# Performance work log

Measured on AMD Instinct MI355X. Metric: run time of the kernel, lower is better.

Reference implementation:

```python
import jax, jax.numpy as jnp
import numpy as np

D_MODEL = 1024
D_STATE = 16
D_CONV = 4
EXPAND = 2
D_INNER = D_MODEL * EXPAND
BATCH = 2
SEQ = 1024


def setup_inputs() -> dict:
    key = jax.random.key(0)
    ks = jax.random.split(key, 9)
    s = lambda fan: 1.0 / np.sqrt(fan)
    x = jax.random.normal(ks[0], (BATCH, SEQ, D_MODEL), jnp.float32)
    W_in = jax.random.normal(ks[1], (D_MODEL, 2 * D_INNER), jnp.float32) * s(D_MODEL)
    conv_w = jax.random.normal(ks[2], (D_INNER, 1, D_CONV), jnp.float32) * s(D_CONV)
    conv_b = jax.random.normal(ks[3], (D_INNER,), jnp.float32) * 0.01
    W_xproj = jax.random.normal(ks[4], (D_INNER, 2 * D_STATE + 1), jnp.float32) * s(D_INNER)
    W_dt = jax.random.normal(ks[5], (1, D_INNER), jnp.float32)
    dt_std = 1.0 / np.sqrt(D_INNER)
    b_dt = jax.random.uniform(ks[6], (D_INNER,), jnp.float32, minval=-dt_std, maxval=dt_std)
    A_log = jnp.log(jnp.arange(1, D_STATE + 1, dtype=jnp.float32))
    Dp = jnp.ones((D_INNER,), jnp.float32)
    W_out = jax.random.normal(ks[7], (D_INNER, D_MODEL), jnp.float32) * s(D_INNER)
    return dict(x=x, W_in=W_in, conv_w=conv_w, conv_b=conv_b, W_xproj=W_xproj,
                W_dt=W_dt, b_dt=b_dt, A_log=A_log, Dp=Dp, W_out=W_out)


def _mamba_forward(x, W_in, conv_w, conv_b, W_xproj, W_dt, b_dt, A_log, Dp, W_out):
    # input projection, split into x branch and gate z
    xz = x @ W_in                              # (B, L, 2*d_inner)
    x_in, z = jnp.split(xz, 2, axis=-1)
    # causal depthwise conv1d: left-pad d_conv-1 (equiv to torch pad=d_conv-1 + truncate to L)
    xc = jnp.transpose(x_in, (0, 2, 1))        # (B, d_inner, L)
    xc = jax.lax.conv_general_dilated(
        xc, conv_w, window_strides=(1,), padding=[(D_CONV - 1, 0)],
        feature_group_count=D_INNER, dimension_numbers=('NCH', 'OIH', 'NCH'))
    xc = xc + conv_b[None, :, None]
    xc = jax.nn.silu(jnp.transpose(xc, (0, 2, 1)))  # (B, L, d_inner)
    # selective SSM
    A = -jnp.exp(A_log)                        # (N,)
    xp = xc @ W_xproj                          # (B, L, 2N+1)
    dt_raw = xp[..., :1]                       # (B, L, 1)
    B_sel = xp[..., 1:1 + D_STATE]             # (B, L, N)
    C_sel = xp[..., 1 + D_STATE:]              # (B, L, N)
    delta = jax.nn.softplus(dt_raw @ W_dt + b_dt)       # (B, L, d_inner)
    dA = jnp.exp(delta[..., None] * A)                   # (B, L, d, N)
    dBx = (delta * xc)[..., None] * B_sel[:, :, None, :]  # (B, L, d, N)

    def step(h, inp):
        dA_t, dBx_t, C_t = inp                 # (B,d,N),(B,d,N),(B,N)
        h = dA_t * h + dBx_t
        y_t = jnp.einsum('bdn,bn->bd', h, C_t)
        return h, y_t

    h0 = jnp.zeros((x.shape[0], D_INNER, D_STATE), xc.dtype)
    _, ys = jax.lax.scan(step, h0,
                         (dA.swapaxes(0, 1), dBx.swapaxes(0, 1), C_sel.swapaxes(0, 1)))
    y = ys.swapaxes(0, 1) + Dp * xc            # (B, L, d_inner)
    y = y * jax.nn.silu(z)
    return y @ W_out                           # (B, L, d_model)


def reference(x, W_in, conv_w, conv_b, W_xproj, W_dt, b_dt, A_log, Dp, W_out):
    return _mamba_forward(x, W_in, conv_w, conv_b, W_xproj, W_dt, b_dt, A_log, Dp, W_out)
```

## Files before the change

### kernel.cpp

```cpp
#include <hip/hip_runtime.h>


#define NTOK   2048
#define NC     64
#define TC     16

typedef unsigned short u16;
typedef short short8 __attribute__((ext_vector_type(8)));
typedef float f32x4 __attribute__((ext_vector_type(4)));

__device__ __forceinline__ float bf2f(u16 v) {
    union { unsigned int u; float f; } w; w.u = ((unsigned int)v) << 16; return w.f;
}
__device__ __forceinline__ u16 f2bf(float f) {
    union { float f; unsigned int u; } w; w.f = f;
    unsigned int u = w.u;
    return (u16)((u + 0x7fffu + ((u >> 16) & 1u)) >> 16);
}

__device__ __forceinline__ void gload_lds16(const u16* g, u16* l) {
    __builtin_amdgcn_global_load_lds(
        (const __attribute__((address_space(1))) void*)g,
        (__attribute__((address_space(3))) void*)l, 16, 0, 0);
}

__device__ __forceinline__ float softplus_f(float x) {
    return fmaxf(x, 0.f) + __logf(1.f + __expf(-__builtin_fabsf(x)));
}

__device__ __forceinline__ void transpose_tile(const float* __restrict__ in,
                                               u16* __restrict__ out,
                                               int R, int C, int n0, int k0,
                                               int tid) {
    __shared__ float tile[32][33];
    const int tx = tid & 31, ty = tid >> 5;
    #pragma unroll
    for (int i = 0; i < 32; i += 8)
        tile[ty + i][tx] = in[(size_t)(k0 + ty + i) * C + n0 + tx];
    __syncthreads();
    #pragma unroll
    for (int i = 0; i < 32; i += 8)
        out[(size_t)(n0 + ty + i) * R + k0 + tx] = f2bf(tile[tx][ty + i]);
}

__global__ __launch_bounds__(256)
void prep_all(const float* __restrict__ x, const float* __restrict__ W_in,
              const float* __restrict__ W_out, const float* __restrict__ W_xproj,
              u16* __restrict__ xbf, u16* __restrict__ WinT,
              u16* __restrict__ WoutT, u16* __restrict__ WxpT) {
    const int tid = threadIdx.x;
    int blk = blockIdx.x;
    if (blk < 8192) {
        int i = blk * 256 + tid;
        xbf[i] = f2bf(x[i]);
        return;
    }
    blk -= 8192;
    if (blk < 4096) {
        transpose_tile(W_in, WinT, 1024, 4096, (blk & 127) * 32, (blk >> 7) * 32, tid);
        return;
    }
    blk -= 4096;
    if (blk < 2048) {
        transpose_tile(W_out, WoutT, 2048, 1024, (blk & 31) * 32, (blk >> 5) * 32, tid);
        return;
    }
    blk -= 2048;
    {
        int gid = blk * 256 + tid;
        int k = gid & 2047;
        int n = gid >> 11;
        WxpT[(size_t)n * 2048 + k] = (n < 33) ? f2bf(W_xproj[(size_t)k * 33 + n]) : (u16)0;
    }
}

template <int OUT_MODE>
__global__ __launch_bounds__(256)
void gemm_bt(const u16* __restrict__ A, const u16* __restrict__ Bt,
             void* __restrict__ Cv, int M, int N, int K) {
    __shared__ __align__(16) u16 As[128 * 32];
    __shared__ __align__(16) u16 Bs[128 * 32];

    const int tid  = threadIdx.x;
    const int lane = tid & 63;
    const int w    = tid >> 6;
    const int wm   = (w >> 1) * 64;
    const int wn   = (w & 1) * 64;
    const int r    = lane & 15;
    const int q    = lane >> 4;
    const int m0   = blockIdx.x * 128;
    const int n0   = blockIdx.y * 128;
    const int kChunk = K / gridDim.z;
    const int k0   = blockIdx.z * kChunk;

    f32x4 acc[4][4];
    #pragma unroll
    for (int i = 0; i < 4; ++i)
        #pragma unroll
        for (int j = 0; j < 4; ++j)
            acc[i][j] = (f32x4){0.f, 0.f, 0.f, 0.f};

    for (int kk = k0; kk < k0 + kChunk; kk += 32) {
        __syncthreads();
        #pragma unroll
        for (int i = 0; i < 2; ++i) {
            int c   = tid + i * 256;
            int row = c >> 2;
            int kc  = (c & 3) << 3;
            int wb  = (i * 256 + (tid & 192)) * 8;
            gload_lds16(&A[(size_t)(m0 + row) * K + kk + kc], &As[wb]);
            gload_lds16(&Bt[(size_t)(n0 + row) * K + kk + kc], &Bs[wb]);
        }
        __syncthreads();

        short8 af[4], bf[4];
        #pragma unroll
        for (int mt = 0; mt < 4; ++mt)
            af[mt] = *(const short8*)(&As[(wm + mt * 16 + r) * 32 + q * 8]);
        #pragma unroll
        for (int nt = 0; nt < 4; ++nt)
            bf[nt] = *(const short8*)(&Bs[(wn + nt * 16 + r) * 32 + q * 8]);

        #pragma unroll
        for (int mt = 0; mt < 4; ++mt)
            #pragma unroll
            for (int nt = 0; nt < 4; ++nt)
                acc[mt][nt] = __builtin_amdgcn_mfma_f32_16x16x32_bf16(
                    af[mt], bf[nt], acc[mt][nt], 0, 0, 0);
    }

    #pragma unroll
    for (int mt = 0; mt < 4; ++mt) {
        #pragma unroll
        for (int nt = 0; nt < 4; ++nt) {
            #pragma unroll
            for (int i = 0; i < 4; ++i) {
                int row = m0 + wm + mt * 16 + q * 4 + i;
                int col = n0 + wn + nt * 16 + r;
                float v = acc[mt][nt][i];
                size_t idx = (size_t)row * N + col;
                if (OUT_MODE == 0) {
                    ((float*)Cv)[idx] = v;
                } else if (OUT_MODE == 1) {
                    atomicAdd(&((float*)Cv)[idx], v);
                } else {
                    ((u16*)Cv)[idx] = f2bf(v);
                }
            }
        }
    }
}

__global__ __launch_bounds__(256)
void conv_silu(const u16* __restrict__ xz, const float* __restrict__ cw,
               const float* __restrict__ cb, u16* __restrict__ xcb) {
    const int d   = blockIdx.x * 256 + threadIdx.x;
    const int tok = blockIdx.y;
    const int b   = tok >> 10;
    const int t   = tok & 1023;
    float s = cb[d];
    #pragma unroll
    for (int k = 0; k < 4; ++k) {
        int tt = t - 3 + k;
        if (tt >= 0)
            s += bf2f(xz[(size_t)(b * 1024 + tt) * 4096 + d]) * cw[d * 4 + k];
    }
    float sl = s / (1.f + __expf(-s));
    xcb[(size_t)tok * 2048 + d] = f2bf(sl);
}

__device__ __forceinline__ void pow_tree(float e1, float* dA) {
    float e2 = e1 * e1, e4 = e2 * e2, e8 = e4 * e4;
    dA[0] = e1;       dA[1] = e2;       dA[2] = e2 * e1;  dA[3] = e4;
    dA[4] = e4 * e1;  dA[5] = e4 * e2;  dA[6] = e4 * dA[2]; dA[7] = e8;
    dA[8] = e8 * e1;  dA[9] = e8 * e2;  dA[10] = e8 * dA[2]; dA[11] = e8 * e4;
    dA[12] = e8 * dA[4]; dA[13] = e8 * dA[5]; dA[14] = e8 * dA[6]; dA[15] = e8 * e8;
}

__global__ __launch_bounds__(256)
void scan_pass1(const u16* __restrict__ xcb, const float* __restrict__ xp,
                const float* __restrict__ W_dt, const float* __restrict__ b_dt,
                const float* __restrict__ A_log,
                float* __restrict__ Sdl, float* __restrict__ hend) {
    const int c  = blockIdx.x;
    const int dg = blockIdx.y;
    const int b  = blockIdx.z;
    const int tid = threadIdx.x;
    const int d  = dg * 256 + tid;
    const int tok0 = b * 1024 + c * TC;

    __shared__ float xps[TC][36];
    for (int e = tid; e < TC * 33; e += 256) {
        int t = (e * 993) >> 15;
        int j = e - t * 33;
        xps[t][j] = xp[(size_t)(tok0 + t) * 128 + j];
    }
    __syncthreads();

    float a[16];
    bool fast = true;
    #pragma unroll
    for (int n = 0; n < 16; ++n) {
        a[n] = -__expf(A_log[n]);
        fast = fast && (__builtin_fabsf(a[n] + (float)(n + 1)) < 1e-3f * (n + 1));
    }

    const float wdt = W_dt[d];
    const float bdt = b_dt[d];

    float h[16];
    #pragma unroll
    for (int n = 0; n < 16; ++n) h[n] = 0.f;
    float sdl = 0.f;

    for (int t = 0; t < TC; ++t) {
        const int tok = tok0 + t;
        const float dl = softplus_f(xps[t][0] * wdt + bdt);
        sdl += dl;
        const float xv = bf2f(xcb[(size_t)tok * 2048 + d]);
        const float wv = dl * xv;
        if (fast) {
            float dA[16];
            pow_tree(__expf(-dl), dA);
            #pragma unroll
            for (int n = 0; n < 16; ++n)
                h[n] = fmaf(dA[n], h[n], wv * xps[t][1 + n]);
        } else {
            #pragma unroll
            for (int n = 0; n < 16; ++n)
                h[n] = fmaf(__expf(dl * a[n]), h[n], wv * xps[t][1 + n]);
        }
    }

    Sdl[(size_t)(b * NC + c) * 2048 + d] = sdl;
    #pragma unroll
    for (int n = 0; n < 16; ++n)
        hend[((size_t)((b * NC + c) * 16 + n)) * 2048 + d] = h[n];
}

__global__ __launch_bounds__(256)
void scan_combine(const float* __restrict__ Sdl, const float* __restrict__ A_log,
                  float* __restrict__ hend) {
    const int gid = blockIdx.x * 256 + threadIdx.x;
    const int d = gid & 2047;
    const int n = (gid >> 11) & 15;
    const int b = gid >> 15;
    const float an = -__expf(A_log[n]);
    float H = 0.f;
    for (int c = 0; c < NC; ++c) {
        size_t cidx = (size_t)(b * NC + c);
        float s  = Sdl[cidx * 2048 + d];
        size_t idx = (cidx * 16 + n) * 2048 + d;
        float he = hend[idx];
        hend[idx] = H;
        H = fmaf(__expf(an * s), H, he);
    }
}

__global__ __launch_bounds__(256)
void scan_pass2(const u16* __restrict__ xcb, const float* __restrict__ xp,
                const float* __restrict__ W_dt, const float* __restrict__ b_dt,
                const float* __restrict__ A_log, const float* __restrict__ Hstart,
                const float* __restrict__ Dp, const u16* __restrict__ xz,
                u16* __restrict__ ybuf) {
    const int c  = blockIdx.x;
    const int dg = blockIdx.y;
    const int b  = blockIdx.z;
    const int tid = threadIdx.x;
    const int d  = dg * 256 + tid;
    const int tok0 = b * 1024 + c * TC;

    __shared__ float xps[TC][36];
    for (int e = tid; e < TC * 33; e += 256) {
        int t = (e * 993) >> 15;
        int j = e - t * 33;
        xps[t][j] = xp[(size_t)(tok0 + t) * 128 + j];
    }
    __syncthreads();

    float a[16];
    bool fast = true;
    #pragma unroll
    for (int n = 0; n < 16; ++n) {
        a[n] = -__expf(A_log[n]);
        fast = fast && (__builtin_fabsf(a[n] + (float)(n + 1)) < 1e-3f * (n + 1));
    }

    const float wdt = W_dt[d];
    const float bdt = b_dt[d];

    float h[16];
    #pragma unroll
    for (int n = 0; n < 16; ++n)
        h[n] = Hstart[((size_t)((b * NC + c) * 16 + n)) * 2048 + d];

    const float Dd = Dp[d];
    for (int t = 0; t < TC; ++t) {
        const int tok = tok0 + t;
        const float dl = softplus_f(xps[t][0] * wdt + bdt);
        const float xv = bf2f(xcb[(size_t)tok * 2048 + d]);
        const float wv = dl * xv;
        if (fast) {
            float dA[16];
            pow_tree(__expf(-dl), dA);
            #pragma unroll
            for (int n = 0; n < 16; ++n)
                h[n] = fmaf(dA[n], h[n], wv * xps[t][1 + n]);
        } else {
            #pragma unroll
            for (int n = 0; n < 16; ++n)
                h[n] = fmaf(__expf(dl * a[n]), h[n], wv * xps[t][1 + n]);
        }
        float y0 = 0.f, y1 = 0.f, y2 = 0.f, y3 = 0.f;
        #pragma unroll
        for (int n = 0; n < 16; n += 4) {
            y0 = fmaf(h[n + 0], xps[t][17 + n + 0], y0);
            y1 = fmaf(h[n + 1], xps[t][17 + n + 1], y1);
            y2 = fmaf(h[n + 2], xps[t][17 + n + 2], y2);
            y3 = fmaf(h[n + 3], xps[t][17 + n + 3], y3);
        }
        float y = (y0 + y1) + (y2 + y3);
        y = fmaf(Dd, xv, y);
        float zv = bf2f(xz[(size_t)tok * 4096 + 2048 + d]);
        float sz = zv / (1.f + __expf(-zv));
        ybuf[(size_t)tok * 2048 + d] = f2bf(y * sz);
    }
}

__global__ void canaries(const float* __restrict__ A_log, float* __restrict__ out,
                         int ws_ok) {
    if (threadIdx.x == 0 && blockIdx.x == 0) {
        float v = A_log[1];
        bool f32ok = (v > 0.683f && v < 0.703f);
        if (!f32ok) out[0] = 400.0f;
        if (!ws_ok) out[0] = 200.0f;
    }
}

extern "C" void kernel_launch(void* const* d_in, const int* in_sizes, int n_in,
                              void* d_out, int out_size, void* d_ws, size_t ws_size,
                              hipStream_t stream) {
    const float* x       = (const float*)d_in[0];
    const float* W_in    = (const float*)d_in[1];
    const float* conv_w  = (const float*)d_in[2];
    const float* conv_b  = (const float*)d_in[3];
    const float* W_xproj = (const float*)d_in[4];
    const float* W_dt    = (const float*)d_in[5];
    const float* b_dt    = (const float*)d_in[6];
    const float* A_log   = (const float*)d_in[7];
    const float* Dp      = (const float*)d_in[8];
    const float* W_out   = (const float*)d_in[9];
    float* out = (float*)d_out;

    char* ws = (char*)d_ws;
    size_t off = 0;
    auto alloc = [&](size_t bytes) -> void* {
        void* p = ws + off;
        off += (bytes + 255) & ~(size_t)255;
        return p;
    };

    u16*   xbf   = (u16*)  alloc((size_t)NTOK * 1024 * 2);
    u16*   xz    = (u16*)  alloc((size_t)NTOK * 4096 * 2);
    u16*   WinT  = (u16*)  alloc((size_t)4096 * 1024 * 2);
    u16*   WoutT = (u16*)  alloc((size_t)1024 * 2048 * 2);
    u16*   WxpT  = (u16*)  alloc((size_t)128 * 2048 * 2);
    u16*   xcb   = (u16*)  alloc((size_t)NTOK * 2048 * 2);
    float* xp    = (float*)alloc((size_t)NTOK * 128 * 4);
    u16*   ybuf  = (u16*)  alloc((size_t)NTOK * 2048 * 2);
    float* Sdl   = (float*)alloc((size_t)2 * NC * 2048 * 4);
    float* hend  = (float*)alloc((size_t)2 * NC * 16 * 2048 * 4);

    const int ws_ok = (off <= ws_size);
    if (ws_ok) {
        hipMemsetAsync(out, 0, (size_t)NTOK * 1024 * 4, stream);
        hipMemsetAsync(xp, 0, (size_t)NTOK * 128 * 4, stream);

        prep_all<<<15360, 256, 0, stream>>>(x, W_in, W_out, W_xproj,
                                            xbf, WinT, WoutT, WxpT);

        gemm_bt<2><<<dim3(16, 32, 1), 256, 0, stream>>>(xbf, WinT, xz,
                                                        2048, 4096, 1024);

        conv_silu<<<dim3(8, NTOK), 256, 0, stream>>>(xz, conv_w, conv_b, xcb);

        gemm_bt<1><<<dim3(16, 1, 8), 256, 0, stream>>>(xcb, WxpT, xp,
                                                       2048, 128, 2048);

        scan_pass1<<<dim3(NC, 8, 2), 256, 0, stream>>>(xcb, xp, W_dt, b_dt, A_log,
                                                       Sdl, hend);
        scan_combine<<<(2 * 16 * 2048) / 256, 256, 0, stream>>>(Sdl, A_log, hend);
        scan_pass2<<<dim3(NC, 8, 2), 256, 0, stream>>>(xcb, xp, W_dt, b_dt, A_log,
                                                       hend, Dp, xz, ybuf);

        gemm_bt<1><<<dim3(16, 8, 4), 256, 0, stream>>>(ybuf, WoutT, out,
                                                       2048, 1024, 2048);
    }

    canaries<<<1, 64, 0, stream>>>(A_log, out, ws_ok);
}
```

Baseline: 252.2 us.

## Replace split-K atomics with partial buffers plus reduction; parallelize chunk-combine scan

The split-K GEMMs now write per-split partial results to separate workspace slices, and a new reduce kernel sums them, replacing atomicAdd and the two memsets. The chunk-combine step of the scan changes from a sequential loop over 64 chunks per thread to a wave-wide Hillis-Steele prefix scan using shuffles, with one wavefront per (b,n,d). This removes atomic contention and the serial dependency chain, at the cost of extra workspace traffic for partials, two extra kernel launches, and a lane-per-chunk layout whose Sdl/hend reads are strided across lanes and therefore uncoalesced.

```diff
diff --git a/kernel.cpp b/kernel.cpp
--- a/kernel.cpp
+++ b/kernel.cpp
@@ -129,6 +129,7 @@
                     af[mt], bf[nt], acc[mt][nt], 0, 0, 0);
     }
 
+    float* Cp = (float*)Cv + (size_t)blockIdx.z * M * N;
     #pragma unroll
     for (int mt = 0; mt < 4; ++mt) {
         #pragma unroll
@@ -140,15 +141,26 @@
                 float v = acc[mt][nt][i];
                 size_t idx = (size_t)row * N + col;
                 if (OUT_MODE == 0) {
-                    ((float*)Cv)[idx] = v;
-                } else if (OUT_MODE == 1) {
-                    atomicAdd(&((float*)Cv)[idx], v);
+                    Cp[idx] = v;
                 } else {
                     ((u16*)Cv)[idx] = f2bf(v);
                 }
             }
         }
     }
+}
+
+__global__ __launch_bounds__(256)
+void reduce_parts(const float4* __restrict__ p, float4* __restrict__ o,
+                  int n4, int parts) {
+    int i = blockIdx.x * 256 + threadIdx.x;
+    if (i >= n4) return;
+    float4 s = p[i];
+    for (int z = 1; z < parts; ++z) {
+        float4 v = p[(size_t)z * n4 + i];
+        s.x += v.x; s.y += v.y; s.z += v.z; s.w += v.w;
+    }
+    o[i] = s;
 }
 
 __global__ __launch_bounds__(256)
@@ -241,20 +253,30 @@
 __global__ __launch_bounds__(256)
 void scan_combine(const float* __restrict__ Sdl, const float* __restrict__ A_log,
                   float* __restrict__ hend) {
-    const int gid = blockIdx.x * 256 + threadIdx.x;
-    const int d = gid & 2047;
-    const int n = (gid >> 11) & 15;
-    const int b = gid >> 15;
+    const int tid  = threadIdx.x;
+    const int lane = tid & 63;
+    const int gw   = blockIdx.x * 4 + (tid >> 6);
+    const int d = gw & 2047;
+    const int n = (gw >> 11) & 15;
+    const int b = gw >> 15;
+
     const float an = -__expf(A_log[n]);
-    float H = 0.f;
-    for (int c = 0; c < NC; ++c) {
-        size_t cidx = (size_t)(b * NC + c);
-        float s  = Sdl[cidx * 2048 + d];
-        size_t idx = (cidx * 16 + n) * 2048 + d;
-        float he = hend[idx];
-        hend[idx] = H;
-        H = fmaf(__expf(an * s), H, he);
-    }
+    const size_t cidx = (size_t)(b * NC + lane);
+    const float s = Sdl[cidx * 2048 + d];
+    const size_t idx = (cidx * 16 + n) * 2048 + d;
+
+    float A = __expf(an * s);
+    float B = hend[idx];
+
+    #pragma unroll
+    for (int st = 1; st < 64; st <<= 1) {
+        float Ao = __shfl_up(A, st, 64);
+        float Bo = __shfl_up(B, st, 64);
+        if (lane >= st) { B = fmaf(A, Bo, B); A = A * Ao; }
+    }
+    float Hs = __shfl_up(B, 1, 64);
+    if (lane == 0) Hs = 0.f;
+    hend[idx] = Hs;
 }
 
 __global__ __launch_bounds__(256)
@@ -366,16 +388,15 @@
     u16*   WoutT = (u16*)  alloc((size_t)1024 * 2048 * 2);
     u16*   WxpT  = (u16*)  alloc((size_t)128 * 2048 * 2);
     u16*   xcb   = (u16*)  alloc((size_t)NTOK * 2048 * 2);
+    float* xpp   = (float*)alloc((size_t)8 * NTOK * 128 * 4);
     float* xp    = (float*)alloc((size_t)NTOK * 128 * 4);
     u16*   ybuf  = (u16*)  alloc((size_t)NTOK * 2048 * 2);
     float* Sdl   = (float*)alloc((size_t)2 * NC * 2048 * 4);
     float* hend  = (float*)alloc((size_t)2 * NC * 16 * 2048 * 4);
+    float* op    = (float*)alloc((size_t)4 * NTOK * 1024 * 4);
 
     const int ws_ok = (off <= ws_size);
     if (ws_ok) {
-        hipMemsetAsync(out, 0, (size_t)NTOK * 1024 * 4, stream);
-        hipMemsetAsync(xp, 0, (size_t)NTOK * 128 * 4, stream);
-
         prep_all<<<15360, 256, 0, stream>>>(x, W_in, W_out, W_xproj,
                                             xbf, WinT, WoutT, WxpT);
 
@@ -384,17 +405,21 @@
 
         conv_silu<<<dim3(8, NTOK), 256, 0, stream>>>(xz, conv_w, conv_b, xcb);
 
-        gemm_bt<1><<<dim3(16, 1, 8), 256, 0, stream>>>(xcb, WxpT, xp,
+        gemm_bt<0><<<dim3(16, 1, 8), 256, 0, stream>>>(xcb, WxpT, xpp,
                                                        2048, 128, 2048);
+        reduce_parts<<<(NTOK * 128 / 4) / 256, 256, 0, stream>>>(
+            (const float4*)xpp, (float4*)xp, NTOK * 128 / 4, 8);
 
         scan_pass1<<<dim3(NC, 8, 2), 256, 0, stream>>>(xcb, xp, W_dt, b_dt, A_log,
                                                        Sdl, hend);
-        scan_combine<<<(2 * 16 * 2048) / 256, 256, 0, stream>>>(Sdl, A_log, hend);
+        scan_combine<<<(2 * 16 * 2048) / 4, 256, 0, stream>>>(Sdl, A_log, hend);
         scan_pass2<<<dim3(NC, 8, 2), 256, 0, stream>>>(xcb, xp, W_dt, b_dt, A_log,
                                                        hend, Dp, xz, ybuf);
 
-        gemm_bt<1><<<dim3(16, 8, 4), 256, 0, stream>>>(ybuf, WoutT, out,
+        gemm_bt<0><<<dim3(16, 8, 4), 256, 0, stream>>>(ybuf, WoutT, op,
                                                        2048, 1024, 2048);
+        reduce_parts<<<(NTOK * 1024 / 4) / 256, 256, 0, stream>>>(
+            (const float4*)op, (float4*)out, NTOK * 1024 / 4, 4);
     }
 
     canaries<<<1, 64, 0, stream>>>(A_log, out, ws_ok);
```

Result: slower. 275.6 us (+9.2%).
